# Kernel tuning notes

Hardware: AMD Instinct MI355X
Metric: run time of the kernel (lower is better)

Reference implementation:

```python
import jax, jax.numpy as jnp
import numpy as np

N = 100000   # local subgraph nodes
E = 600000   # directed edges
D = 128      # memory_dim
B = 10000    # label nodes queried
C = 32       # num_classes


def _glorot(key, shape):
    s = 1.0 / np.sqrt(shape[0])
    return jax.random.uniform(key, shape, jnp.float32, -s, s)


def setup_inputs() -> dict:
    key = jax.random.key(0)
    ks = jax.random.split(key, 16)
    return {
        "node_state": jax.random.normal(ks[0], (N, D), jnp.float32),
        "edge_index": jax.random.randint(ks[1], (2, E), 0, N),
        "label_pos": jax.random.randint(ks[2], (B,), 0, N),
        # SAGEConv 1: lin_l (neighbor, with bias), lin_r (root, no bias)
        "W1l": _glorot(ks[3], (D, D)), "b1l": jnp.zeros((D,), jnp.float32),
        "W1r": _glorot(ks[4], (D, D)),
        # SAGEConv 2
        "W2l": _glorot(ks[5], (D, D)), "b2l": jnp.zeros((D,), jnp.float32),
        "W2r": _glorot(ks[6], (D, D)),
        # classifier: Linear(D,D) -> ReLU -> Linear(D,C)
        "Wc1": _glorot(ks[7], (D, D)), "bc1": jnp.zeros((D,), jnp.float32),
        "Wc2": _glorot(ks[8], (D, C)), "bc2": jnp.zeros((C,), jnp.float32),
    }


def _sage(x, src, dst, Wl, bl, Wr):
    # PyG SAGEConv, aggr='mean': out_i = lin_l(mean_{j: (j->i)} x_j) + lin_r(x_i)
    n = x.shape[0]
    agg = jax.ops.segment_sum(x[src], dst, num_segments=n)          # [N, D]
    cnt = jax.ops.segment_sum(jnp.ones_like(dst, x.dtype), dst, num_segments=n)
    mean = agg / jnp.maximum(cnt, 1.0)[:, None]
    return mean @ Wl + bl + x @ Wr


def reference(node_state, edge_index, label_pos,
              W1l, b1l, W1r, W2l, b2l, W2r, Wc1, bc1, Wc2, bc2):
    src, dst = edge_index[0], edge_index[1]
    x = jax.nn.relu(_sage(node_state, src, dst, W1l, b1l, W1r))
    x = jax.nn.relu(_sage(x, src, dst, W2l, b2l, W2r))
    h = jax.nn.relu(x[label_pos] @ Wc1 + bc1)                        # [B, D]
    return h @ Wc2 + bc2                                             # [B, C]
```

## Files before the change

kernel.cpp:

```cpp
#include <hip/hip_runtime.h>
#include <hip/hip_bf16.h>

static constexpr int N = 100000;
static constexpr int E = 600000;
static constexpr int D = 128;
static constexpr int B = 10000;
static constexpr int C = 32;

typedef __attribute__((ext_vector_type(8))) short short8;
typedef __attribute__((ext_vector_type(4))) float f32x4;

static __device__ __forceinline__ unsigned short f2bf(float f) {
    unsigned u = __float_as_uint(f);
    unsigned r = (u + 0x7FFFu + ((u >> 16) & 1u)) >> 16;
    return (unsigned short)r;
}
static __device__ __forceinline__ float bf2f(unsigned short h) {
    return __uint_as_float(((unsigned)h) << 16);
}

static __device__ __forceinline__ void split8(const float4 v0, const float4 v1,
                                              short8& h, short8& l) {
    const float f[8] = {v0.x, v0.y, v0.z, v0.w, v1.x, v1.y, v1.z, v1.w};
    #pragma unroll
    for (int i = 0; i < 8; ++i) {
        unsigned short hh = f2bf(f[i]);
        h[i] = (short)hh;
        l[i] = (short)f2bf(f[i] - bf2f(hh));
    }
}


__global__ void deg_k(const int* __restrict__ dst, int* __restrict__ deg, int nE) {
    int i = blockIdx.x * blockDim.x + threadIdx.x;
    if (i < nE) atomicAdd(&deg[dst[i]], 1);
}

__global__ __launch_bounds__(256) void scan1_k(const int* __restrict__ v,
                                               int* __restrict__ bsum, int n) {
    __shared__ int lsum[256];
    const int t = threadIdx.x;
    const int base = blockIdx.x * 1024 + t * 4;
    int s = 0;
    #pragma unroll
    for (int i = 0; i < 4; ++i) {
        int idx = base + i;
        if (idx < n) s += v[idx];
    }
    lsum[t] = s;
    __syncthreads();
    for (int off = 128; off > 0; off >>= 1) {
        if (t < off) lsum[t] += lsum[t + off];
        __syncthreads();
    }
    if (t == 0) bsum[blockIdx.x] = lsum[0];
}

__global__ __launch_bounds__(128) void scan2_k(const int* __restrict__ bsum,
                                               int* __restrict__ boff,
                                               int* __restrict__ total, int nb) {
    __shared__ int s[128];
    const int t = threadIdx.x;
    const int v = (t < nb) ? bsum[t] : 0;
    s[t] = v;
    __syncthreads();
    for (int off = 1; off < 128; off <<= 1) {
        int u = (t >= off) ? s[t - off] : 0;
        __syncthreads();
        s[t] += u;
        __syncthreads();
    }
    if (t < nb) boff[t] = s[t] - v;
    if (t == 127) *total = s[127];
}

__global__ __launch_bounds__(256) void scan3_k(const int* __restrict__ deg,
                                               const int* __restrict__ boff,
                                               int* __restrict__ roff,
                                               int* __restrict__ cur, int n) {
    __shared__ int lsum[256];
    const int t = threadIdx.x;
    const int base = blockIdx.x * 1024 + t * 4;
    int d[4];
    int s = 0;
    #pragma unroll
    for (int i = 0; i < 4; ++i) {
        int idx = base + i;
        d[i] = (idx < n) ? deg[idx] : 0;
        s += d[i];
    }
    lsum[t] = s;
    __syncthreads();
    for (int off = 1; off < 256; off <<= 1) {
        int u = (t >= off) ? lsum[t - off] : 0;
        __syncthreads();
        lsum[t] += u;
        __syncthreads();
    }
    int run = boff[blockIdx.x] + lsum[t] - s;
    #pragma unroll
    for (int i = 0; i < 4; ++i) {
        int idx = base + i;
        if (idx < n) {
            roff[idx] = run;
            cur[idx]  = run;
            run += d[i];
        }
    }
}

__global__ void fill_k(const int* __restrict__ src, const int* __restrict__ dst,
                       int* __restrict__ cur, int* __restrict__ csr_src, int nE) {
    int e = blockIdx.x * blockDim.x + threadIdx.x;
    if (e < nE) {
        int p = atomicAdd(&cur[dst[e]], 1);
        csr_src[p] = src[e];
    }
}

__global__ __launch_bounds__(256) void mark_k(
    const int* __restrict__ label_pos, const int* __restrict__ roff,
    const int* __restrict__ csr_src, int* __restrict__ flag, int nlab) {
    const int w = blockIdx.x * (blockDim.x >> 6) + (threadIdx.x >> 6);
    if (w >= nlab) return;
    const int lane = threadIdx.x & 63;
    const int v = label_pos[w];
    if (lane == 0) flag[v] = 1;
    const int jb = roff[v], je = roff[v + 1];
    for (int j = jb + lane; j < je; j += 64) flag[csr_src[j]] = 1;
}

__global__ __launch_bounds__(256) void uscan3_k(const int* __restrict__ flag,
                                                const int* __restrict__ boff,
                                                int* __restrict__ map,
                                                int* __restrict__ ulist, int n) {
    __shared__ int lsum[256];
    const int t = threadIdx.x;
    const int base = blockIdx.x * 1024 + t * 4;
    int f[4];
    int s = 0;
    #pragma unroll
    for (int i = 0; i < 4; ++i) {
        int idx = base + i;
        f[i] = (idx < n) ? flag[idx] : 0;
        s += f[i];
    }
    lsum[t] = s;
    __syncthreads();
    for (int off = 1; off < 256; off <<= 1) {
        int u = (t >= off) ? lsum[t - off] : 0;
        __syncthreads();
        lsum[t] += u;
        __syncthreads();
    }
    int run = boff[blockIdx.x] + lsum[t] - s;
    #pragma unroll
    for (int i = 0; i < 4; ++i) {
        int idx = base + i;
        if (idx < n && f[i]) {
            map[idx] = run;
            ulist[run] = idx;
            ++run;
        }
    }
}

__global__ __launch_bounds__(256) void swz_k(const float* W0, const float* W1,
                                             const float* W2, const float* W3,
                                             unsigned short* __restrict__ out) {
    const int m = blockIdx.x >> 4;
    const int chunk = blockIdx.x & 15;
    const float* W = (m == 0) ? W0 : (m == 1) ? W1 : (m == 2) ? W2 : W3;
    unsigned short* o = out + (size_t)m * 32768;
    #pragma unroll
    for (int it = 0; it < 4; ++it) {
        int f = chunk * 1024 + it * 256 + threadIdx.x;
        int j = f & 7;
        int lane = (f >> 3) & 63;
        int fi = f >> 9;
        int k = (fi >> 3) * 32 + (lane >> 4) * 8 + j;
        int n = (fi & 7) * 16 + (lane & 15);
        float a = W[k * 128 + n];
        unsigned short h = f2bf(a);
        unsigned short l = f2bf(a - bf2f(h));
        o[f] = h;
        o[16384 + f] = l;
    }
}

template <bool GATHER, bool MAP>
__global__ __launch_bounds__(256) void gather_mean_k(
    const float* __restrict__ x, const int* __restrict__ roff,
    const int* __restrict__ csr_src, const int* __restrict__ rows,
    const int* __restrict__ map, const int* __restrict__ nrows_ptr,
    float* __restrict__ out, int nrows_max) {
    const int nrows = nrows_ptr ? nrows_ptr[0] : nrows_max;
    const int w = blockIdx.x * (blockDim.x >> 6) + (threadIdx.x >> 6);
    if (w >= nrows) return;
    const int lane = threadIdx.x & 63;
    const int n  = GATHER ? rows[w] : w;
    const int jb = roff[n];
    const int je = roff[n + 1];
    const float* xb = x + lane * 2;

    float ax = 0.f, ay = 0.f;
    int j = jb;
    for (; j + 4 <= je; j += 4) {
        int s0 = csr_src[j + 0];
        int s1 = csr_src[j + 1];
        int s2 = csr_src[j + 2];
        int s3 = csr_src[j + 3];
        if (MAP) { s0 = map[s0]; s1 = map[s1]; s2 = map[s2]; s3 = map[s3]; }
        float2 v0 = *reinterpret_cast<const float2*>(xb + (size_t)s0 * D);
        float2 v1 = *reinterpret_cast<const float2*>(xb + (size_t)s1 * D);
        float2 v2 = *reinterpret_cast<const float2*>(xb + (size_t)s2 * D);
        float2 v3 = *reinterpret_cast<const float2*>(xb + (size_t)s3 * D);
        ax += v0.x + v1.x + v2.x + v3.x;
        ay += v0.y + v1.y + v2.y + v3.y;
    }
    for (; j < je; ++j) {
        int s = csr_src[j];
        if (MAP) s = map[s];
        float2 v = *reinterpret_cast<const float2*>(xb + (size_t)s * D);
        ax += v.x;
        ay += v.y;
    }
    const float inv = 1.0f / fmaxf((float)(je - jb), 1.0f);
    *reinterpret_cast<float2*>(out + (size_t)w * D + lane * 2) =
        make_float2(ax * inv, ay * inv);
}

template <bool GATHER, bool MAP>
__global__ __launch_bounds__(256, 6) void sage_mfma_k(
    const float* __restrict__ mean, const float* __restrict__ xsrc,
    const int* __restrict__ rows, const int* __restrict__ map,
    const int* __restrict__ nrows_ptr,
    const unsigned short* __restrict__ WlSw, const unsigned short* __restrict__ WrSw,
    const float* __restrict__ bl, float* __restrict__ xout, int nrows_max)
{
    const int nrows = nrows_ptr ? nrows_ptr[0] : nrows_max;
    const int rb = blockIdx.x * 32;
    if (rb >= nrows) return;

    const int t = threadIdx.x;
    const int wrow = (t >> 6) & 1;
    const int wcol = t >> 7;
    const int lane = t & 63;
    const int mcol = lane & 15;
    const int q = lane >> 4;
    const int r = rb + wrow * 16 + mcol;

    f32x4 acc[4];
    #pragma unroll
    for (int no = 0; no < 4; ++no) acc[no] = (f32x4){0.f, 0.f, 0.f, 0.f};

    size_t gidx = 0;
    if (r < nrows) {
        int g = GATHER ? rows[r] : r;
        if (MAP) g = map[g];
        gidx = (size_t)g;
    }

    #pragma unroll
    for (int br = 0; br < 2; ++br) {
        const unsigned short* __restrict__ Wm = br ? WrSw : WlSw;
        #pragma unroll
        for (int kp = 0; kp < 4; ++kp) {
            short8 aH, aL;
            {
                float4 v0 = make_float4(0.f, 0.f, 0.f, 0.f);
                float4 v1 = make_float4(0.f, 0.f, 0.f, 0.f);
                if (r < nrows) {
                    const float* p = (br == 0)
                        ? mean + (size_t)r * D + kp * 32 + q * 8
                        : xsrc + gidx * D + kp * 32 + q * 8;
                    v0 = *reinterpret_cast<const float4*>(p);
                    v1 = *reinterpret_cast<const float4*>(p + 4);
                }
                split8(v0, v1, aH, aL);
            }
            #pragma unroll
            for (int no = 0; no < 4; ++no) {
                const size_t fo = ((size_t)(kp * 8 + wcol * 4 + no) * 64 + lane) * 8;
                short8 bh = *reinterpret_cast<const short8*>(Wm + fo);
                short8 bo = *reinterpret_cast<const short8*>(Wm + 16384 + fo);
                acc[no] = __builtin_amdgcn_mfma_f32_16x16x32_bf16(aH, bh, acc[no], 0, 0, 0);
                acc[no] = __builtin_amdgcn_mfma_f32_16x16x32_bf16(aL, bh, acc[no], 0, 0, 0);
                acc[no] = __builtin_amdgcn_mfma_f32_16x16x32_bf16(aH, bo, acc[no], 0, 0, 0);
            }
        }
    }

    #pragma unroll
    for (int no = 0; no < 4; ++no) {
        const int col = wcol * 64 + no * 16 + mcol;
        const float bias = bl[col];
        #pragma unroll
        for (int ri = 0; ri < 4; ++ri) {
            const int row = rb + wrow * 16 + q * 4 + ri;
            if (row < nrows)
                xout[(size_t)row * D + col] = fmaxf(acc[no][ri] + bias, 0.f);
        }
    }
}

__global__ __launch_bounds__(256) void classifier_k(
    const float* __restrict__ x2g,
    const float* __restrict__ Wc1, const float* __restrict__ bc1,
    const float* __restrict__ Wc2, const float* __restrict__ bc2,
    float* __restrict__ out, int nrows) {
    __shared__ float Xs[32][128];
    __shared__ float Hs[32][128];
    const int rb = blockIdx.x * 32;
    const int t  = threadIdx.x;

    #pragma unroll
    for (int it = 0; it < 4; ++it) {
        int j  = t + it * 256;
        int r  = j >> 5;
        int k4 = j & 31;
        int row = rb + r;
        float4 v = make_float4(0.f, 0.f, 0.f, 0.f);
        if (row < nrows) v = *reinterpret_cast<const float4*>(x2g + (size_t)row * D + k4 * 4);
        *reinterpret_cast<float4*>(&Xs[r][k4 * 4]) = v;
    }
    __syncthreads();

    {
        const int col  = t & 127;
        const int half = t >> 7;
        float acc[16];
        const float bias = bc1[col];
        #pragma unroll
        for (int i = 0; i < 16; ++i) acc[i] = bias;
        for (int k = 0; k < 128; ++k) {
            float w = Wc1[k * 128 + col];
            #pragma unroll
            for (int i = 0; i < 16; ++i)
                acc[i] = fmaf(Xs[half * 16 + i][k], w, acc[i]);
        }
        #pragma unroll
        for (int i = 0; i < 16; ++i)
            Hs[half * 16 + i][col] = fmaxf(acc[i], 0.0f);
    }
    __syncthreads();

    {
        const int c  = t & 31;
        const int rg = t >> 5;
        float o[4];
        const float b2 = bc2[c];
        #pragma unroll
        for (int i = 0; i < 4; ++i) o[i] = b2;
        for (int k = 0; k < 128; ++k) {
            float w = Wc2[k * 32 + c];
            #pragma unroll
            for (int i = 0; i < 4; ++i)
                o[i] = fmaf(Hs[rg + 8 * i][k], w, o[i]);
        }
        #pragma unroll
        for (int i = 0; i < 4; ++i) {
            int row = rb + rg + 8 * i;
            if (row < nrows) out[(size_t)row * C + c] = o[i];
        }
    }
}


extern "C" void kernel_launch(void* const* d_in, const int* in_sizes, int n_in,
                              void* d_out, int out_size, void* d_ws, size_t ws_size,
                              hipStream_t stream) {
    const float* node_state = (const float*)d_in[0];
    const int*   edge_index = (const int*)d_in[1];
    const int*   label_pos  = (const int*)d_in[2];
    const float* W1l = (const float*)d_in[3];
    const float* b1l = (const float*)d_in[4];
    const float* W1r = (const float*)d_in[5];
    const float* W2l = (const float*)d_in[6];
    const float* b2l = (const float*)d_in[7];
    const float* W2r = (const float*)d_in[8];
    const float* Wc1 = (const float*)d_in[9];
    const float* bc1 = (const float*)d_in[10];
    const float* Wc2 = (const float*)d_in[11];
    const float* bc2 = (const float*)d_in[12];
    float* out = (float*)d_out;

    const int* src = edge_index;
    const int* dst = edge_index + E;

    char* ws = (char*)d_ws;
    float* x1c   = (float*)ws;                    ws += sizeof(float) * (size_t)N * D;
    float* bufA  = (float*)ws;                    ws += sizeof(float) * (size_t)N * D;
    unsigned short* Wsw = (unsigned short*)ws;    ws += sizeof(unsigned short) * 4 * 32768;
    int* deg     = (int*)ws;                      ws += sizeof(int) * N;
    int* flag    = (int*)ws;                      ws += sizeof(int) * N;
    int* roff    = (int*)ws;                      ws += sizeof(int) * (N + 1);
    int* cur     = (int*)ws;                      ws += sizeof(int) * N;
    int* csr_src = (int*)ws;                      ws += sizeof(int) * E;
    int* map     = (int*)ws;                      ws += sizeof(int) * N;
    int* ulist   = (int*)ws;                      ws += sizeof(int) * N;
    int* bsum    = (int*)ws;                      ws += sizeof(int) * 128;
    int* boff    = (int*)ws;                      ws += sizeof(int) * 128;
    int* ucnt    = (int*)ws;                      ws += sizeof(int);
    float* mean1c = bufA;
    float* mean2g = bufA;
    float* x2g    = bufA + (size_t)B * D;

    const int TB = 256;
    const int NB = (N + 1023) / 1024;

    hipMemsetAsync(deg, 0, sizeof(int) * 2 * N, stream);
    deg_k<<<(E + TB - 1) / TB, TB, 0, stream>>>(dst, deg, E);
    scan1_k<<<NB, 256, 0, stream>>>(deg, bsum, N);
    scan2_k<<<1, 128, 0, stream>>>(bsum, boff, roff + N, NB);
    scan3_k<<<NB, 256, 0, stream>>>(deg, boff, roff, cur, N);
    fill_k<<<(E + TB - 1) / TB, TB, 0, stream>>>(src, dst, cur, csr_src, E);

    mark_k<<<(B + 3) / 4, TB, 0, stream>>>(label_pos, roff, csr_src, flag, B);
    scan1_k<<<NB, 256, 0, stream>>>(flag, bsum, N);
    scan2_k<<<1, 128, 0, stream>>>(bsum, boff, ucnt, NB);
    uscan3_k<<<NB, 256, 0, stream>>>(flag, boff, map, ulist, N);

    swz_k<<<64, 256, 0, stream>>>(W1l, W1r, W2l, W2r, Wsw);

    gather_mean_k<true, false><<<(N + 3) / 4, TB, 0, stream>>>(
        node_state, roff, csr_src, ulist, nullptr, ucnt, mean1c, N);
    sage_mfma_k<true, false><<<(N + 31) / 32, TB, 0, stream>>>(
        mean1c, node_state, ulist, nullptr, ucnt,
        Wsw, Wsw + 32768, b1l, x1c, N);

    gather_mean_k<true, true><<<(B + 3) / 4, TB, 0, stream>>>(
        x1c, roff, csr_src, label_pos, map, nullptr, mean2g, B);
    sage_mfma_k<true, true><<<(B + 31) / 32, TB, 0, stream>>>(
        mean2g, x1c, label_pos, map, nullptr,
        Wsw + 65536, Wsw + 98304, b2l, x2g, B);

    classifier_k<<<(B + 31) / 32, TB, 0, stream>>>(x2g, Wc1, bc1, Wc2, bc2, out, B);
}
```

Before: 286.5 us.

## Cut kernel launches by fusing preprocessing and using atomic node compaction

Fuses the degree-count kernel with the weight swizzle kernel, folds the block-offset scan into scan3 (each block rescans the block sums), and replaces the flag scan/compaction pipeline with atomicCAS plus an atomic counter inside the marking kernel. This removes five kernel launches and the serialized small scan kernels. The cost is that the compacted node order becomes nondeterministic and hurts gather locality, and contention on one global counter may be heavy with many unique nodes.

```diff
diff --git a/kernel.cpp b/kernel.cpp
--- a/kernel.cpp
+++ b/kernel.cpp
@@ -6,6 +6,7 @@
 static constexpr int D = 128;
 static constexpr int B = 10000;
 static constexpr int C = 32;
+static constexpr int NB = (N + 1023) / 1024;
 
 typedef __attribute__((ext_vector_type(8))) short short8;
 typedef __attribute__((ext_vector_type(4))) float f32x4;
@@ -30,146 +31,18 @@
     }
 }
 
-
-__global__ void deg_k(const int* __restrict__ dst, int* __restrict__ deg, int nE) {
-    int i = blockIdx.x * blockDim.x + threadIdx.x;
-    if (i < nE) atomicAdd(&deg[dst[i]], 1);
-}
-
-__global__ __launch_bounds__(256) void scan1_k(const int* __restrict__ v,
-                                               int* __restrict__ bsum, int n) {
-    __shared__ int lsum[256];
-    const int t = threadIdx.x;
-    const int base = blockIdx.x * 1024 + t * 4;
-    int s = 0;
-    #pragma unroll
-    for (int i = 0; i < 4; ++i) {
-        int idx = base + i;
-        if (idx < n) s += v[idx];
-    }
-    lsum[t] = s;
-    __syncthreads();
-    for (int off = 128; off > 0; off >>= 1) {
-        if (t < off) lsum[t] += lsum[t + off];
-        __syncthreads();
-    }
-    if (t == 0) bsum[blockIdx.x] = lsum[0];
-}
-
-__global__ __launch_bounds__(128) void scan2_k(const int* __restrict__ bsum,
-                                               int* __restrict__ boff,
-                                               int* __restrict__ total, int nb) {
-    __shared__ int s[128];
-    const int t = threadIdx.x;
-    const int v = (t < nb) ? bsum[t] : 0;
-    s[t] = v;
-    __syncthreads();
-    for (int off = 1; off < 128; off <<= 1) {
-        int u = (t >= off) ? s[t - off] : 0;
-        __syncthreads();
-        s[t] += u;
-        __syncthreads();
-    }
-    if (t < nb) boff[t] = s[t] - v;
-    if (t == 127) *total = s[127];
-}
-
-__global__ __launch_bounds__(256) void scan3_k(const int* __restrict__ deg,
-                                               const int* __restrict__ boff,
-                                               int* __restrict__ roff,
-                                               int* __restrict__ cur, int n) {
-    __shared__ int lsum[256];
-    const int t = threadIdx.x;
-    const int base = blockIdx.x * 1024 + t * 4;
-    int d[4];
-    int s = 0;
-    #pragma unroll
-    for (int i = 0; i < 4; ++i) {
-        int idx = base + i;
-        d[i] = (idx < n) ? deg[idx] : 0;
-        s += d[i];
-    }
-    lsum[t] = s;
-    __syncthreads();
-    for (int off = 1; off < 256; off <<= 1) {
-        int u = (t >= off) ? lsum[t - off] : 0;
-        __syncthreads();
-        lsum[t] += u;
-        __syncthreads();
-    }
-    int run = boff[blockIdx.x] + lsum[t] - s;
-    #pragma unroll
-    for (int i = 0; i < 4; ++i) {
-        int idx = base + i;
-        if (idx < n) {
-            roff[idx] = run;
-            cur[idx]  = run;
-            run += d[i];
-        }
-    }
-}
-
-__global__ void fill_k(const int* __restrict__ src, const int* __restrict__ dst,
-                       int* __restrict__ cur, int* __restrict__ csr_src, int nE) {
-    int e = blockIdx.x * blockDim.x + threadIdx.x;
-    if (e < nE) {
-        int p = atomicAdd(&cur[dst[e]], 1);
-        csr_src[p] = src[e];
-    }
-}
-
-__global__ __launch_bounds__(256) void mark_k(
-    const int* __restrict__ label_pos, const int* __restrict__ roff,
-    const int* __restrict__ csr_src, int* __restrict__ flag, int nlab) {
-    const int w = blockIdx.x * (blockDim.x >> 6) + (threadIdx.x >> 6);
-    if (w >= nlab) return;
-    const int lane = threadIdx.x & 63;
-    const int v = label_pos[w];
-    if (lane == 0) flag[v] = 1;
-    const int jb = roff[v], je = roff[v + 1];
-    for (int j = jb + lane; j < je; j += 64) flag[csr_src[j]] = 1;
-}
-
-__global__ __launch_bounds__(256) void uscan3_k(const int* __restrict__ flag,
-                                                const int* __restrict__ boff,
-                                                int* __restrict__ map,
-                                                int* __restrict__ ulist, int n) {
-    __shared__ int lsum[256];
-    const int t = threadIdx.x;
-    const int base = blockIdx.x * 1024 + t * 4;
-    int f[4];
-    int s = 0;
-    #pragma unroll
-    for (int i = 0; i < 4; ++i) {
-        int idx = base + i;
-        f[i] = (idx < n) ? flag[idx] : 0;
-        s += f[i];
-    }
-    lsum[t] = s;
-    __syncthreads();
-    for (int off = 1; off < 256; off <<= 1) {
-        int u = (t >= off) ? lsum[t - off] : 0;
-        __syncthreads();
-        lsum[t] += u;
-        __syncthreads();
-    }
-    int run = boff[blockIdx.x] + lsum[t] - s;
-    #pragma unroll
-    for (int i = 0; i < 4; ++i) {
-        int idx = base + i;
-        if (idx < n && f[i]) {
-            map[idx] = run;
-            ulist[run] = idx;
-            ++run;
-        }
-    }
-}
-
-__global__ __launch_bounds__(256) void swz_k(const float* W0, const float* W1,
-                                             const float* W2, const float* W3,
-                                             unsigned short* __restrict__ out) {
-    const int m = blockIdx.x >> 4;
-    const int chunk = blockIdx.x & 15;
+__global__ __launch_bounds__(256) void deg_swz_k(
+    const int* __restrict__ dst, int* __restrict__ deg, int nE, int EB,
+    const float* W0, const float* W1, const float* W2, const float* W3,
+    unsigned short* __restrict__ out) {
+    if ((int)blockIdx.x < EB) {
+        int i = blockIdx.x * 256 + threadIdx.x;
+        if (i < nE) atomicAdd(&deg[dst[i]], 1);
+        return;
+    }
+    const int sb = blockIdx.x - EB;
+    const int m = sb >> 4;
+    const int chunk = sb & 15;
     const float* W = (m == 0) ? W0 : (m == 1) ? W1 : (m == 2) ? W2 : W3;
     unsigned short* o = out + (size_t)m * 32768;
     #pragma unroll
@@ -182,9 +55,111 @@
         int n = (fi & 7) * 16 + (lane & 15);
         float a = W[k * 128 + n];
         unsigned short h = f2bf(a);
-        unsigned short l = f2bf(a - bf2f(h));
         o[f] = h;
-        o[16384 + f] = l;
+        o[16384 + f] = f2bf(a - bf2f(h));
+    }
+}
+
+__global__ __launch_bounds__(256) void scan1_k(const int* __restrict__ v,
+                                               int* __restrict__ bsum, int n) {
+    __shared__ int lsum[256];
+    const int t = threadIdx.x;
+    const int base = blockIdx.x * 1024 + t * 4;
+    int s = 0;
+    #pragma unroll
+    for (int i = 0; i < 4; ++i) {
+        int idx = base + i;
+        if (idx < n) s += v[idx];
+    }
+    lsum[t] = s;
+    __syncthreads();
+    for (int off = 128; off > 0; off >>= 1) {
+        if (t < off) lsum[t] += lsum[t + off];
+        __syncthreads();
+    }
+    if (t == 0) bsum[blockIdx.x] = lsum[0];
+}
+
+__global__ __launch_bounds__(256) void scan3_k(const int* __restrict__ deg,
+                                               const int* __restrict__ bsum,
+                                               int* __restrict__ roff,
+                                               int* __restrict__ cur, int n) {
+    __shared__ int sb[128];
+    __shared__ int lsum[256];
+    const int t = threadIdx.x;
+    if (t < 128) sb[t] = (t < NB) ? bsum[t] : 0;
+    __syncthreads();
+    for (int off = 1; off < 128; off <<= 1) {
+        int u = (t < 128 && t >= off) ? sb[t - off] : 0;
+        __syncthreads();
+        if (t < 128) sb[t] += u;
+        __syncthreads();
+    }
+    const int boff = (blockIdx.x == 0) ? 0 : sb[blockIdx.x - 1];
+    if (blockIdx.x == 0 && t == 0) roff[n] = sb[NB - 1];
+
+    const int base = blockIdx.x * 1024 + t * 4;
+    int d[4];
+    int s = 0;
+    #pragma unroll
+    for (int i = 0; i < 4; ++i) {
+        int idx = base + i;
+        d[i] = (idx < n) ? deg[idx] : 0;
+        s += d[i];
+    }
+    lsum[t] = s;
+    __syncthreads();
+    for (int off = 1; off < 256; off <<= 1) {
+        int u = (t >= off) ? lsum[t - off] : 0;
+        __syncthreads();
+        lsum[t] += u;
+        __syncthreads();
+    }
+    int run = boff + lsum[t] - s;
+    #pragma unroll
+    for (int i = 0; i < 4; ++i) {
+        int idx = base + i;
+        if (idx < n) {
+            roff[idx] = run;
+            cur[idx]  = run;
+            run += d[i];
+        }
+    }
+}
+
+__global__ void fill_k(const int* __restrict__ src, const int* __restrict__ dst,
+                       int* __restrict__ cur, int* __restrict__ csr_src, int nE) {
+    int e = blockIdx.x * blockDim.x + threadIdx.x;
+    if (e < nE) {
+        int p = atomicAdd(&cur[dst[e]], 1);
+        csr_src[p] = src[e];
+    }
+}
+
+__global__ __launch_bounds__(256) void mark2_k(
+    const int* __restrict__ label_pos, const int* __restrict__ roff,
+    const int* __restrict__ csr_src, int* __restrict__ flag,
+    int* __restrict__ map, int* __restrict__ ulist, int* __restrict__ ucnt,
+    int nlab) {
+    const int w = blockIdx.x * (blockDim.x >> 6) + (threadIdx.x >> 6);
+    if (w >= nlab) return;
+    const int lane = threadIdx.x & 63;
+    const int v = label_pos[w];
+    if (lane == 0) {
+        if (atomicCAS(&flag[v], 0, 1) == 0) {
+            int p = atomicAdd(ucnt, 1);
+            map[v] = p;
+            ulist[p] = v;
+        }
+    }
+    const int jb = roff[v], je = roff[v + 1];
+    for (int j = jb + lane; j < je; j += 64) {
+        int u = csr_src[j];
+        if (atomicCAS(&flag[u], 0, 1) == 0) {
+            int p = atomicAdd(ucnt, 1);
+            map[u] = p;
+            ulist[p] = u;
+        }
     }
 }
 
@@ -394,34 +369,29 @@
     unsigned short* Wsw = (unsigned short*)ws;    ws += sizeof(unsigned short) * 4 * 32768;
     int* deg     = (int*)ws;                      ws += sizeof(int) * N;
     int* flag    = (int*)ws;                      ws += sizeof(int) * N;
+    int* ucnt    = (int*)ws;                      ws += sizeof(int);
+    ws += sizeof(int) * 3;
     int* roff    = (int*)ws;                      ws += sizeof(int) * (N + 1);
     int* cur     = (int*)ws;                      ws += sizeof(int) * N;
     int* csr_src = (int*)ws;                      ws += sizeof(int) * E;
     int* map     = (int*)ws;                      ws += sizeof(int) * N;
     int* ulist   = (int*)ws;                      ws += sizeof(int) * N;
     int* bsum    = (int*)ws;                      ws += sizeof(int) * 128;
-    int* boff    = (int*)ws;                      ws += sizeof(int) * 128;
-    int* ucnt    = (int*)ws;                      ws += sizeof(int);
     float* mean1c = bufA;
     float* mean2g = bufA;
     float* x2g    = bufA + (size_t)B * D;
 
     const int TB = 256;
-    const int NB = (N + 1023) / 1024;
-
-    hipMemsetAsync(deg, 0, sizeof(int) * 2 * N, stream);
-    deg_k<<<(E + TB - 1) / TB, TB, 0, stream>>>(dst, deg, E);
+    const int EB = (E + TB - 1) / TB;
+
+    hipMemsetAsync(deg, 0, sizeof(int) * (2 * N + 1), stream);
+    deg_swz_k<<<EB + 64, TB, 0, stream>>>(dst, deg, E, EB,
+                                          W1l, W1r, W2l, W2r, Wsw);
     scan1_k<<<NB, 256, 0, stream>>>(deg, bsum, N);
-    scan2_k<<<1, 128, 0, stream>>>(bsum, boff, roff + N, NB);
-    scan3_k<<<NB, 256, 0, stream>>>(deg, boff, roff, cur, N);
-    fill_k<<<(E + TB - 1) / TB, TB, 0, stream>>>(src, dst, cur, csr_src, E);
-
-    mark_k<<<(B + 3) / 4, TB, 0, stream>>>(label_pos, roff, csr_src, flag, B);
-    scan1_k<<<NB, 256, 0, stream>>>(flag, bsum, N);
-    scan2_k<<<1, 128, 0, stream>>>(bsum, boff, ucnt, NB);
-    uscan3_k<<<NB, 256, 0, stream>>>(flag, boff, map, ulist, N);
-
-    swz_k<<<64, 256, 0, stream>>>(W1l, W1r, W2l, W2r, Wsw);
+    scan3_k<<<NB, 256, 0, stream>>>(deg, bsum, roff, cur, N);
+    fill_k<<<EB, TB, 0, stream>>>(src, dst, cur, csr_src, E);
+    mark2_k<<<(B + 3) / 4, TB, 0, stream>>>(label_pos, roff, csr_src,
+                                            flag, map, ulist, ucnt, B);
 
     gather_mean_k<true, false><<<(N + 3) / 4, TB, 0, stream>>>(
         node_state, roff, csr_src, ulist, nullptr, ucnt, mean1c, N);
```

Measured after the change: 487.1 us. +70.0%, slower.
